# Kernel tuning notes

Measured on AMD Instinct MI355X. Metric: run time of the kernel, lower is better.

## Reference

```python
import jax, jax.numpy as jnp
import numpy as np

NUM_NODES = 100
WINDOW = 128
GH = 256       # graph_hidden_channels
DH = 64        # discrepancy_hidden_channels
OUT = 128      # out_channels
B = 256        # graphs per batch
N = B * NUM_NODES
E = 409600


def _mconv(x, w, b):
    # x: [B, n, W], w: [n, 2, k], b: [n, 2]  (per-node Conv1d(1,2,k), 'same' padding)
    k = w.shape[-1]
    W = x.shape[-1]
    p = k // 2
    xp = jnp.pad(x, ((0, 0), (0, 0), (p, p)))
    win = jnp.stack([xp[..., j:j + W] for j in range(k)], axis=-1)  # [B,n,W,k]
    return jnp.einsum('bnwk,nck->bncw', win, w) + b[None, :, :, None]


def _gcn(x, edge_index, Wg, bg):
    # PyG GCNConv: add self-loops, symmetric normalization, then linear
    Nn = x.shape[0]
    xw = x @ Wg.T
    loops = jnp.arange(Nn, dtype=edge_index.dtype)
    src = jnp.concatenate([edge_index[0], loops])
    dst = jnp.concatenate([edge_index[1], loops])
    deg = jax.ops.segment_sum(jnp.ones(src.shape[0], dtype=xw.dtype), dst, num_segments=Nn)
    norm = jax.lax.rsqrt(jnp.maximum(deg, 1e-12))
    coef = norm[src] * norm[dst]
    agg = jax.ops.segment_sum(coef[:, None] * xw[src], dst, num_segments=Nn)
    return agg + bg


def setup_inputs() -> dict:
    key = jax.random.key(0)
    ks = jax.random.split(key, 20)
    f = 6 * WINDOW
    s = lambda d: 1.0 / np.sqrt(d)
    inp = {
        'x1': jax.random.normal(ks[0], (N, WINDOW), jnp.float32),
        'x2': jax.random.normal(ks[1], (N, WINDOW), jnp.float32),
        'edge_index1': jax.random.randint(ks[2], (2, E), 0, N, jnp.int32),
        'edge_index2': jax.random.randint(ks[3], (2, E), 0, N, jnp.int32),
        'w3': jax.random.normal(ks[4], (NUM_NODES, 2, 3), jnp.float32) * s(3),
        'b3': jax.random.normal(ks[5], (NUM_NODES, 2), jnp.float32) * s(3),
        'w5': jax.random.normal(ks[6], (NUM_NODES, 2, 5), jnp.float32) * s(5),
        'b5': jax.random.normal(ks[7], (NUM_NODES, 2), jnp.float32) * s(5),
        'w7': jax.random.normal(ks[8], (NUM_NODES, 2, 7), jnp.float32) * s(7),
        'b7': jax.random.normal(ks[9], (NUM_NODES, 2), jnp.float32) * s(7),
        'Wff': jax.random.normal(ks[10], (NUM_NODES, GH, f), jnp.float32) * s(f),
        'bff': jax.random.normal(ks[11], (NUM_NODES, GH), jnp.float32) * s(f),
        'Wg': jax.random.normal(ks[12], (GH, GH), jnp.float32) * s(GH),
        'bg': jax.random.normal(ks[13], (GH,), jnp.float32) * s(GH),
        'Wd': jax.random.normal(ks[14], (NUM_NODES, DH, 2 * GH), jnp.float32) * s(2 * GH),
        'bd': jax.random.normal(ks[15], (NUM_NODES, DH), jnp.float32) * s(2 * GH),
        'Wfc': jax.random.normal(ks[16], (OUT, NUM_NODES * DH), jnp.float32) * s(NUM_NODES * DH),
        'bfc': jax.random.normal(ks[17], (OUT,), jnp.float32) * s(NUM_NODES * DH),
    }
    return inp


def reference(x1, x2, edge_index1, edge_index2, w3, b3, w5, b5, w7, b7,
              Wff, bff, Wg, bg, Wd, bd, Wfc, bfc):
    n = w3.shape[0]
    Nn, W = x1.shape
    Bg = Nn // n

    def branch(x):
        xg = x.reshape(Bg, n, W)
        # multiscale CNN: concat conv3/conv5/conv7 along channel -> [B,n,6,W]
        c = jnp.concatenate([_mconv(xg, w3, b3), _mconv(xg, w5, b5), _mconv(xg, w7, b7)], axis=2)
        c = jax.nn.relu(c.reshape(Bg, n, 6 * W))            # channel-major flatten (matches view(-1))
        h = jax.nn.relu(jnp.einsum('bnf,nhf->bnh', c, Wff) + bff)
        return h.reshape(Nn, -1)

    h1 = jax.nn.relu(_gcn(branch(x1), edge_index1, Wg, bg))
    h2 = jax.nn.relu(_gcn(branch(x2), edge_index2, Wg, bg))
    H = h1.shape[-1]
    cat = jnp.concatenate([h1.reshape(Bg, n, H), h2.reshape(Bg, n, H)], axis=-1)  # [B,n,2H]
    d = jnp.einsum('bnf,ndf->bnd', cat, Wd) + bd            # per-node discrepancy FC
    du = jax.nn.relu(d.reshape(Bg, -1))                     # node-major -> [B, n*DH]
    return du @ Wfc.T + bfc
```

## Files before the change

kernel.cpp:

```cpp
#include <hip/hip_runtime.h>

#define DI __device__ __forceinline__

typedef __bf16 bf16_t;
typedef bf16_t bf16x8 __attribute__((ext_vector_type(8)));
typedef float f32x4 __attribute__((ext_vector_type(4)));
typedef ushort ushort8v __attribute__((ext_vector_type(8)));

static constexpr int NNODE = 100, WIN = 128, GH = 256, DH = 64, OUTC = 128, NB = 256;
static constexpr int NTOT = NB * NNODE;
static constexpr int NE = 409600;
static constexpr int FFK = 6 * WIN;
static constexpr size_t CB = (size_t)NNODE * NB * FFK;
static constexpr size_t HB = (size_t)NTOT * GH;
static constexpr int CVT_BLKS = 23264;
static constexpr int NSEG = 64, SEGE = NE / NSEG;
static constexpr int NPK = NTOT / 2;

DI ushort f2bf(float f) {
  union { float f; unsigned u; } v; v.f = f;
  unsigned r = v.u + 0x7fffu + ((v.u >> 16) & 1u);
  return (ushort)(r >> 16);
}
DI float bf2f(ushort s) {
  union { unsigned u; float f; } v; v.u = ((unsigned)s) << 16; return v.f;
}

DI void gload16(const void* g, void* l) {
  __builtin_amdgcn_global_load_lds((const __attribute__((address_space(1))) void*)g,
                                   (__attribute__((address_space(3))) void*)l, 16, 0, 0);
}


DI void cvt_body(int bx, const float* s0, const float* s1, const float* s2, const float* s3,
                 ushort* d0, ushort* d1, ushort* d2, ushort* d3) {
  int j = bx * 256 + threadIdx.x;
  const float* s; ushort* d;
  if (j < 19660800 / 4) { s = s0; d = d0; }
  else if ((j -= 19660800 / 4) < 3276800 / 4) { s = s1; d = d1; }
  else if ((j -= 3276800 / 4) < 819200 / 4) { s = s2; d = d2; }
  else { j -= 819200 / 4; s = s3; d = d3; }
  float4 v = reinterpret_cast<const float4*>(s)[j];
  ushort4 o;
  o.x = f2bf(v.x); o.y = f2bf(v.y); o.z = f2bf(v.z); o.w = f2bf(v.w);
  reinterpret_cast<ushort4*>(d)[j] = o;
}

DI void histseg_body(int bx, const int* e1d, const int* e2d,
                     ushort* rank_local, uint* segcnt, uint* cnt ) {
  int set = bx & 1, seg = bx >> 1;
  int tid = threadIdx.x;
#pragma unroll
  for (int k = 0; k < NPK / 256; ++k) cnt[tid + k * 256] = 0;
  __syncthreads();
  const int* dstp = (set ? e2d : e1d) + seg * SEGE;
  ushort* rl = rank_local + set * NE + seg * SEGE;
#pragma unroll
  for (int k = 0; k < SEGE / 256; ++k) {
    int i = k * 256 + tid;
    int d = dstp[i];
    uint sh = (d & 1) * 16;
    uint old = atomicAdd(&cnt[d >> 1], 1u << sh);
    rl[i] = (ushort)((old >> sh) & 0xffffu);
  }
  __syncthreads();
  uint* sc = segcnt + (size_t)(set * NSEG + seg) * NPK;
#pragma unroll
  for (int k = 0; k < NPK / 256; ++k) sc[tid + k * 256] = cnt[tid + k * 256];
}

DI void fill_body(int bx, const int* e1, const int* e2, const int* offs,
                  const ushort* rank_local, const uint* segbase, int* csr) {
  int i = bx * 256 + threadIdx.x;
  int set = i >= NE;
  int ii = i - set * NE;
  const int* e = set ? e2 : e1;
  int d = e[NE + ii];
  int seg = ii / SEGE;
  uint b32 = segbase[(size_t)(set * NSEG + seg) * NPK + (d >> 1)];
  int base = (b32 >> ((d & 1) * 16)) & 0xffff;
  int pos = offs[set * (NTOT + 1) + d] + base + rank_local[i];
  csr[set * NE + pos] = e[ii];
}

DI void scan_body(int set, const int* deg_, int* offs_, float* norm_) {
  const int* deg = deg_ + set * NTOT;
  int* offs = offs_ + set * (NTOT + 1);
  float* norm = norm_ + set * NTOT;
  __shared__ int part[256];
  int t = threadIdx.x;
  int base = t * 100;
  int s = 0;
  for (int j = 0; j < 100; ++j) s += deg[base + j];
  part[t] = s;
  __syncthreads();
  for (int d = 1; d < 256; d <<= 1) {
    int vv = (t >= d) ? part[t - d] : 0;
    __syncthreads();
    part[t] += vv;
    __syncthreads();
  }
  int run = (t > 0) ? part[t - 1] : 0;
  for (int j = 0; j < 100; ++j) {
    int dv = deg[base + j];
    offs[base + j] = run;
    norm[base + j] = rsqrtf((float)(dv + 1));
    run += dv;
  }
  if (t == 255) offs[NTOT] = part[255];
}

DI void conv_body(int bx, const float* x1, const float* x2,
                  const float* w3, const float* b3, const float* w5, const float* b5,
                  const float* w7, const float* b7, ushort* c, float* xs ) {
  const int t = threadIdx.x;
  const int rowi = t >> 4;
  const int idx = t & 15;
  int r = bx * 16 + rowi;
  int br = r >= NTOT;
  int rr = r - br * NTOT;
  const float* x = br ? x2 : x1;
  int b = rr / 100, node = rr - b * 100;

  float* row = xs + rowi * 136;
  const int w0 = idx * 8;
  float4 v0 = *reinterpret_cast<const float4*>(x + (size_t)rr * WIN + w0);
  float4 v1 = *reinterpret_cast<const float4*>(x + (size_t)rr * WIN + w0 + 4);
  *reinterpret_cast<float4*>(&row[4 + w0]) = v0;
  *reinterpret_cast<float4*>(&row[4 + w0 + 4]) = v1;
  if (idx == 0) { row[0] = 0.f; row[1] = 0.f; row[2] = 0.f; row[3] = 0.f; }
  if (idx == 15) { row[132] = 0.f; row[133] = 0.f; row[134] = 0.f; row[135] = 0.f; }
  __syncthreads();

  float xv[14];
#pragma unroll
  for (int j = 0; j < 14; ++j) xv[j] = row[1 + w0 + j];

  const float* W3 = w3 + node * 6;  const float* B3 = b3 + node * 2;
  const float* W5 = w5 + node * 10; const float* B5 = b5 + node * 2;
  const float* W7 = w7 + node * 14; const float* B7 = b7 + node * 2;
  ushort* out = c + (size_t)br * CB + (size_t)(node * NB + b) * FFK + w0;

#pragma unroll
  for (int ch = 0; ch < 2; ++ch) {
    float k3[3], k5[5], k7[7];
#pragma unroll
    for (int j = 0; j < 3; ++j) k3[j] = W3[ch * 3 + j];
#pragma unroll
    for (int j = 0; j < 5; ++j) k5[j] = W5[ch * 5 + j];
#pragma unroll
    for (int j = 0; j < 7; ++j) k7[j] = W7[ch * 7 + j];
    float bb3 = B3[ch], bb5 = B5[ch], bb7 = B7[ch];
    ushort8v o3, o5, o7;
#pragma unroll
    for (int p = 0; p < 8; ++p) {
      float a3 = bb3, a5 = bb5, a7 = bb7;
#pragma unroll
      for (int j = 0; j < 3; ++j) a3 += k3[j] * xv[p + 2 + j];
#pragma unroll
      for (int j = 0; j < 5; ++j) a5 += k5[j] * xv[p + 1 + j];
#pragma unroll
      for (int j = 0; j < 7; ++j) a7 += k7[j] * xv[p + j];
      o3[p] = f2bf(fmaxf(a3, 0.f));
      o5[p] = f2bf(fmaxf(a5, 0.f));
      o7[p] = f2bf(fmaxf(a7, 0.f));
    }
    *reinterpret_cast<ushort8v*>(out + (0 + ch) * WIN) = o3;
    *reinterpret_cast<ushort8v*>(out + (2 + ch) * WIN) = o5;
    *reinterpret_cast<ushort8v*>(out + (4 + ch) * WIN) = o7;
  }
}

template <int MODE>
DI void gemm_body(int bx, int by, const ushort* __restrict__ A, const ushort* __restrict__ A2,
                  const ushort* __restrict__ Bm, ushort* __restrict__ obf,
                  float* __restrict__ of, const float* __restrict__ bias) {
  constexpr int BN = (MODE == 2) ? 64 : 128;
  constexpr int KT = (MODE == 0) ? 12 : (MODE == 1) ? 4 : (MODE == 2) ? 8 : 4;
  constexpr int LDA = (MODE == 0) ? 768 : (MODE == 1) ? 256 : (MODE == 2) ? 256 : 6400;
  constexpr int LDB = (MODE == 0) ? 768 : (MODE == 1) ? 256 : (MODE == 2) ? 512 : 6400;
  constexpr int MF = (MODE == 2) ? 2 : 4;
  constexpr int NF = 4;

  __shared__ ushort As[128 * 64];
  __shared__ ushort Bs[BN * 64];

  const int tid = threadIdx.x, wv = tid >> 6, lane = tid & 63;
  const int j8 = (((lane & 7) ^ (lane >> 3)) - (lane & 7)) * 8;

  int mt = 0, nt = 0, node = 0, kbase = 0, br = 0;
  if constexpr (MODE == 0) {
    int h = bx;
    int s = (h & 7) * 100 + (h >> 3);
    nt = s & 1; int rest = s >> 1;
    mt = rest & 1; int yy = rest >> 1;
    br = yy >= 100; node = yy - br * 100;
  } else if constexpr (MODE == 1) {
    int h = bx;
    int s = (h & 7) * 100 + (h >> 3);
    nt = s & 1; int rest = s >> 1;
    br = rest >= 200; mt = rest - br * 200;
  } else if constexpr (MODE == 2) { mt = bx; node = by; }
  else { mt = bx; kbase = by * 256; }

  const ushort* Ab = nullptr; const ushort* Bb = nullptr;
  if constexpr (MODE == 0) { Ab = A + (size_t)br * CB + (size_t)node * (NB * FFK) + (size_t)mt * 128 * FFK;
                             Bb = Bm + (size_t)node * (GH * FFK) + (size_t)nt * 128 * FFK; }
  else if constexpr (MODE == 1) { Ab = A + (size_t)br * HB + (size_t)mt * 128 * GH;
                                  Bb = Bm + (size_t)nt * 128 * GH; }
  else if constexpr (MODE == 2) { Bb = Bm + (size_t)node * (DH * 512); }
  else { Ab = A + (size_t)mt * 128 * 6400 + kbase; Bb = Bm + kbase; }

  const int wr = (MODE == 2) ? wv : (wv >> 1);
  const int wc = (MODE == 2) ? 0 : (wv & 1);

  f32x4 acc[MF][NF] = {};

  for (int kt = 0; kt < KT; ++kt) {
    const int k0 = kt * 64;
    __syncthreads();
#pragma unroll
    for (int it = 0; it < 4; ++it) {
      int rb = it * 32 + wv * 8;
      int row = rb + (lane >> 3);
      const ushort* gp;
      if constexpr (MODE == 2) {
        int b_ = mt * 128 + row;
        const ushort* src = (k0 < 256) ? A : A2;
        gp = src + (size_t)(b_ * NNODE + node) * GH + (k0 & 255) + (lane & 7) * 8 + j8;
      } else {
        gp = Ab + (size_t)row * LDA + k0 + (lane & 7) * 8 + j8;
      }
      gload16(gp, &As[rb * 64]);
    }
#pragma unroll
    for (int it = 0; it < BN / 32; ++it) {
      int rb = it * 32 + wv * 8;
      int row = rb + (lane >> 3);
      gload16(Bb + (size_t)row * LDB + k0 + (lane & 7) * 8 + j8, &Bs[rb * 64]);
    }
    __syncthreads();
#pragma unroll
    for (int kk = 0; kk < 2; ++kk) {
      const int ch8 = ((kk * 4 + (lane >> 4)) ^ (lane & 7)) * 8;
      bf16x8 af[MF], bfr[NF];
#pragma unroll
      for (int m = 0; m < MF; ++m) {
        int rr = wr * (MF * 16) + m * 16 + (lane & 15);
        af[m] = *reinterpret_cast<const bf16x8*>(&As[rr * 64 + ch8]);
      }
#pragma unroll
      for (int n = 0; n < NF; ++n) {
        int rr = wc * 64 + n * 16 + (lane & 15);
        bfr[n] = *reinterpret_cast<const bf16x8*>(&Bs[rr * 64 + ch8]);
      }
#pragma unroll
      for (int m = 0; m < MF; ++m)
#pragma unroll
        for (int n = 0; n < NF; ++n)
          acc[m][n] = __builtin_amdgcn_mfma_f32_16x16x32_bf16(af[m], bfr[n], acc[m][n], 0, 0, 0);
    }
  }

  const int lrow = (lane >> 4) * 4, lcol = lane & 15;
#pragma unroll
  for (int m = 0; m < MF; ++m) {
#pragma unroll
    for (int n = 0; n < NF; ++n) {
      int cc = wc * 64 + n * 16 + lcol;
#pragma unroll
      for (int rg = 0; rg < 4; ++rg) {
        int rr = wr * (MF * 16) + m * 16 + lrow + rg;
        float val = acc[m][n][rg];
        if constexpr (MODE == 0) {
          int b_ = mt * 128 + rr;
          int col = nt * 128 + cc;
          val = fmaxf(val + bias[node * GH + col], 0.f);
          obf[(size_t)br * HB + (size_t)(b_ * NNODE + node) * GH + col] = f2bf(val);
        } else if constexpr (MODE == 1) {
          int R = mt * 128 + rr;
          int col = nt * 128 + cc;
          obf[(size_t)br * HB + (size_t)R * GH + col] = f2bf(val * bias[br * NTOT + R]);
        } else if constexpr (MODE == 2) {
          int b_ = mt * 128 + rr;
          val = fmaxf(val + bias[node * DH + cc], 0.f);
          obf[(size_t)b_ * (NNODE * DH) + node * DH + cc] = f2bf(val);
        } else {
          int R = mt * 128 + rr;
          if (by == 0) val += bias[cc];
          atomicAdd(&of[R * OUTC + cc], val);
        }
      }
    }
  }
}


__global__ __launch_bounds__(256) void fused1_k(
    const float* __restrict__ Wff, const float* __restrict__ Wd,
    const float* __restrict__ Wfc, const float* __restrict__ Wg,
    ushort* __restrict__ Wffb, ushort* __restrict__ Wdb,
    ushort* __restrict__ Wfcb, ushort* __restrict__ Wgb,
    const int* __restrict__ e1d, const int* __restrict__ e2d,
    ushort* __restrict__ rank_local, uint* __restrict__ segcnt,
    const float* __restrict__ x1, const float* __restrict__ x2,
    const float* __restrict__ w3, const float* __restrict__ b3,
    const float* __restrict__ w5, const float* __restrict__ b5,
    const float* __restrict__ w7, const float* __restrict__ b7,
    ushort* __restrict__ c) {
  __shared__ uint smem[NPK];
  int bx = blockIdx.x;
  if (bx < 128) histseg_body(bx, e1d, e2d, rank_local, segcnt, smem);
  else if (bx < 3328) conv_body(bx - 128, x1, x2, w3, b3, w5, b5, w7, b7, c, (float*)smem);
  else cvt_body(bx - 3328, Wff, Wd, Wfc, Wg, Wffb, Wdb, Wfcb, Wgb);
}

__global__ __launch_bounds__(256) void segscan_k(const uint* __restrict__ segcnt,
                                                 uint* __restrict__ segbase, int* __restrict__ deg) {
  int set = blockIdx.y;
  int p = blockIdx.x * 256 + threadIdx.x;
  uint lo = 0, hi = 0;
  const uint* sc = segcnt + (size_t)set * NSEG * NPK + p;
  uint* sb = segbase + (size_t)set * NSEG * NPK + p;
  for (int s = 0; s < NSEG; ++s) {
    uint v = sc[(size_t)s * NPK];
    sb[(size_t)s * NPK] = lo | (hi << 16);
    lo += v & 0xffffu; hi += v >> 16;
  }
  reinterpret_cast<int2*>(deg)[set * NPK + p] = make_int2((int)lo, (int)hi);
}

__global__ __launch_bounds__(256) void scan_k(const int* __restrict__ deg,
                                              int* __restrict__ offs, float* __restrict__ nrm) {
  scan_body(blockIdx.x, deg, offs, nrm);
}

__global__ __launch_bounds__(256) void fused3_k(
    const ushort* __restrict__ cbuf, const ushort* __restrict__ Wffb,
    ushort* __restrict__ h, const float* __restrict__ bff,
    const int* __restrict__ e1, const int* __restrict__ e2,
    const int* __restrict__ offs, const ushort* __restrict__ rank_local,
    const uint* __restrict__ segbase, int* __restrict__ csr) {
  if ((int)blockIdx.x < 800)
    gemm_body<0>(blockIdx.x, 0, cbuf, nullptr, Wffb, h, nullptr, bff);
  else
    fill_body(blockIdx.x - 800, e1, e2, offs, rank_local, segbase, csr);
}

template <int MODE>
__global__ __launch_bounds__(256) void gemm_k(const ushort* __restrict__ A, const ushort* __restrict__ A2,
                                              const ushort* __restrict__ Bm, ushort* __restrict__ obf,
                                              float* __restrict__ of, const float* __restrict__ bias) {
  gemm_body<MODE>(blockIdx.x, blockIdx.y, A, A2, Bm, obf, of, bias);
}

__global__ __launch_bounds__(256) void agg_k(const ushort* __restrict__ xw_, const int* __restrict__ offs_,
                                             const int* __restrict__ csr_, const float* __restrict__ norm_,
                                             const float* __restrict__ bg, ushort* __restrict__ hg_) {
  int idx = blockIdx.x * 4 + (threadIdx.x >> 6);
  int br = idx >= NTOT;
  int v = idx - br * NTOT;
  const ushort* xw = xw_ + (size_t)br * HB;
  const int* offs = offs_ + br * (NTOT + 1);
  const int* csr = csr_ + br * NE;
  const float* norm = norm_ + br * NTOT;
  ushort* hg = hg_ + (size_t)br * HB;

  int lane = threadIdx.x & 63;
  int half = lane >> 5;
  int colb = (lane & 31) * 8;
  const ushort* base = xw + colb;

  float a[8] = {0.f, 0.f, 0.f, 0.f, 0.f, 0.f, 0.f, 0.f};
  if (half == 0) {
    ushort8v q = *reinterpret_cast<const ushort8v*>(base + (size_t)v * GH);
#pragma unroll
    for (int i = 0; i < 8; ++i) a[i] += bf2f(q[i]);
  }
  int e0 = offs[v], e1 = offs[v + 1];
  int j = e0 + half;
  for (; j + 6 < e1; j += 8) {
    int s0 = csr[j], s1 = csr[j + 2], s2 = csr[j + 4], s3 = csr[j + 6];
    ushort8v q0 = *reinterpret_cast<const ushort8v*>(base + (size_t)s0 * GH);
    ushort8v q1 = *reinterpret_cast<const ushort8v*>(base + (size_t)s1 * GH);
    ushort8v q2 = *reinterpret_cast<const ushort8v*>(base + (size_t)s2 * GH);
    ushort8v q3 = *reinterpret_cast<const ushort8v*>(base + (size_t)s3 * GH);
#pragma unroll
    for (int i = 0; i < 8; ++i)
      a[i] += (bf2f(q0[i]) + bf2f(q1[i])) + (bf2f(q2[i]) + bf2f(q3[i]));
  }
  for (; j + 2 < e1; j += 4) {
    int s0 = csr[j], s1 = csr[j + 2];
    ushort8v q0 = *reinterpret_cast<const ushort8v*>(base + (size_t)s0 * GH);
    ushort8v q1 = *reinterpret_cast<const ushort8v*>(base + (size_t)s1 * GH);
#pragma unroll
    for (int i = 0; i < 8; ++i) a[i] += bf2f(q0[i]) + bf2f(q1[i]);
  }
  if (j < e1) {
    int s0 = csr[j];
    ushort8v q0 = *reinterpret_cast<const ushort8v*>(base + (size_t)s0 * GH);
#pragma unroll
    for (int i = 0; i < 8; ++i) a[i] += bf2f(q0[i]);
  }
#pragma unroll
  for (int i = 0; i < 8; ++i) a[i] += __shfl_xor(a[i], 32);

  if (half == 0) {
    float nv = norm[v];
    float4 bb0 = *reinterpret_cast<const float4*>(bg + colb);
    float4 bb1 = *reinterpret_cast<const float4*>(bg + colb + 4);
    ushort8v o;
    o[0] = f2bf(fmaxf(nv * a[0] + bb0.x, 0.f));
    o[1] = f2bf(fmaxf(nv * a[1] + bb0.y, 0.f));
    o[2] = f2bf(fmaxf(nv * a[2] + bb0.z, 0.f));
    o[3] = f2bf(fmaxf(nv * a[3] + bb0.w, 0.f));
    o[4] = f2bf(fmaxf(nv * a[4] + bb1.x, 0.f));
    o[5] = f2bf(fmaxf(nv * a[5] + bb1.y, 0.f));
    o[6] = f2bf(fmaxf(nv * a[6] + bb1.z, 0.f));
    o[7] = f2bf(fmaxf(nv * a[7] + bb1.w, 0.f));
    *reinterpret_cast<ushort8v*>(hg + (size_t)v * GH + colb) = o;
  }
}

extern "C" void kernel_launch(void* const* d_in, const int* in_sizes, int n_in,
                              void* d_out, int out_size, void* d_ws, size_t ws_size,
                              hipStream_t stream) {
  const float* x1 = (const float*)d_in[0];
  const float* x2 = (const float*)d_in[1];
  const int* e1 = (const int*)d_in[2];
  const int* e2 = (const int*)d_in[3];
  const float* w3 = (const float*)d_in[4];  const float* b3 = (const float*)d_in[5];
  const float* w5 = (const float*)d_in[6];  const float* b5 = (const float*)d_in[7];
  const float* w7 = (const float*)d_in[8];  const float* b7 = (const float*)d_in[9];
  const float* Wff = (const float*)d_in[10]; const float* bff = (const float*)d_in[11];
  const float* Wg = (const float*)d_in[12];  const float* bg = (const float*)d_in[13];
  const float* Wd = (const float*)d_in[14];  const float* bd = (const float*)d_in[15];
  const float* Wfc = (const float*)d_in[16]; const float* bfc = (const float*)d_in[17];
  float* out = (float*)d_out;

  char* ws = (char*)d_ws;
  size_t off = 0;
  auto alloc = [&](size_t bytes) -> char* {
    char* p = ws + off;
    off = (off + bytes + 255) & ~(size_t)255;
    return p;
  };
  ushort* Wffb = (ushort*)alloc(19660800ull * 2);
  ushort* Wdb  = (ushort*)alloc(3276800ull * 2);
  ushort* Wfcb = (ushort*)alloc(819200ull * 2);
  ushort* Wgb  = (ushort*)alloc(65536ull * 2);
  ushort* cbuf = (ushort*)alloc(2 * CB * 2);
  ushort* h    = (ushort*)alloc(2 * HB * 2);
  ushort* xw   = (ushort*)alloc(2 * HB * 2);
  int* deg     = (int*)alloc(2 * NTOT * 4);
  int* offs    = (int*)alloc(2 * (NTOT + 1) * 4);
  ushort* rankl = (ushort*)alloc(2 * NE * 2);
  uint* segcnt  = (uint*)alloc((size_t)2 * NSEG * NPK * 4);
  uint* segbase = (uint*)alloc((size_t)2 * NSEG * NPK * 4);
  int* csr     = (int*)alloc(2 * NE * 4);
  float* nrm   = (float*)alloc(2 * NTOT * 4);
  ushort* du = cbuf;

  hipMemsetAsync(out, 0, (size_t)out_size * 4, stream);

  fused1_k<<<128 + 3200 + CVT_BLKS, 256, 0, stream>>>(
      Wff, Wd, Wfc, Wg, Wffb, Wdb, Wfcb, Wgb,
      e1 + NE, e2 + NE, rankl, segcnt,
      x1, x2, w3, b3, w5, b5, w7, b7, cbuf);
  segscan_k<<<dim3(NPK / 256, 2), 256, 0, stream>>>(segcnt, segbase, deg);
  scan_k<<<2, 256, 0, stream>>>(deg, offs, nrm);
  fused3_k<<<4000, 256, 0, stream>>>(cbuf, Wffb, h, bff, e1, e2, offs, rankl, segbase, csr);

  gemm_k<1><<<800, 256, 0, stream>>>(h, nullptr, Wgb, xw, nullptr, nrm);
  agg_k<<<12800, 256, 0, stream>>>(xw, offs, csr, nrm, bg, h);

  gemm_k<2><<<dim3(2, 100), 256, 0, stream>>>(h, h + HB, Wdb, du, nullptr, bd);
  gemm_k<3><<<dim3(2, 25), 256, 0, stream>>>(du, nullptr, Wfcb, nullptr, out, bfc);
}
```

Measured before the change: 252.1 us.

## Split GCN aggregation into column slices with half-wave per node

The aggregation kernel now splits the 256 feature columns into four 64-column slices handled by separate blocks, each half-wave processing one node with 4-byte gathers instead of 16-byte gathers split across two half-waves. Block indexing interleaves the branch and slice so neighboring blocks share the same node range, aiming for better L2 locality and more parallelism per edge list. The cost is re-reading CSR indices four times and much narrower memory transactions per gathered row.

```diff
diff --git a/kernel.cpp b/kernel.cpp
--- a/kernel.cpp
+++ b/kernel.cpp
@@ -357,69 +357,47 @@
 __global__ __launch_bounds__(256) void agg_k(const ushort* __restrict__ xw_, const int* __restrict__ offs_,
                                              const int* __restrict__ csr_, const float* __restrict__ norm_,
                                              const float* __restrict__ bg, ushort* __restrict__ hg_) {
-  int idx = blockIdx.x * 4 + (threadIdx.x >> 6);
-  int br = idx >= NTOT;
-  int v = idx - br * NTOT;
+  int bid = blockIdx.x;
+  int c = bid & 7;
+  int i = bid >> 3;
+  int br = c >> 2, slice = c & 3;
+  int hw = threadIdx.x >> 5;
+  int v = i * 8 + hw;
+  int l = threadIdx.x & 31;
+  int col = slice * 64 + l * 2;
+
   const ushort* xw = xw_ + (size_t)br * HB;
   const int* offs = offs_ + br * (NTOT + 1);
   const int* csr = csr_ + br * NE;
   const float* norm = norm_ + br * NTOT;
   ushort* hg = hg_ + (size_t)br * HB;
-
-  int lane = threadIdx.x & 63;
-  int half = lane >> 5;
-  int colb = (lane & 31) * 8;
-  const ushort* base = xw + colb;
-
-  float a[8] = {0.f, 0.f, 0.f, 0.f, 0.f, 0.f, 0.f, 0.f};
-  if (half == 0) {
-    ushort8v q = *reinterpret_cast<const ushort8v*>(base + (size_t)v * GH);
-#pragma unroll
-    for (int i = 0; i < 8; ++i) a[i] += bf2f(q[i]);
-  }
-  int e0 = offs[v], e1 = offs[v + 1];
-  int j = e0 + half;
-  for (; j + 6 < e1; j += 8) {
-    int s0 = csr[j], s1 = csr[j + 2], s2 = csr[j + 4], s3 = csr[j + 6];
-    ushort8v q0 = *reinterpret_cast<const ushort8v*>(base + (size_t)s0 * GH);
-    ushort8v q1 = *reinterpret_cast<const ushort8v*>(base + (size_t)s1 * GH);
-    ushort8v q2 = *reinterpret_cast<const ushort8v*>(base + (size_t)s2 * GH);
-    ushort8v q3 = *reinterpret_cast<const ushort8v*>(base + (size_t)s3 * GH);
-#pragma unroll
-    for (int i = 0; i < 8; ++i)
-      a[i] += (bf2f(q0[i]) + bf2f(q1[i])) + (bf2f(q2[i]) + bf2f(q3[i]));
-  }
-  for (; j + 2 < e1; j += 4) {
-    int s0 = csr[j], s1 = csr[j + 2];
-    ushort8v q0 = *reinterpret_cast<const ushort8v*>(base + (size_t)s0 * GH);
-    ushort8v q1 = *reinterpret_cast<const ushort8v*>(base + (size_t)s1 * GH);
-#pragma unroll
-    for (int i = 0; i < 8; ++i) a[i] += bf2f(q0[i]) + bf2f(q1[i]);
-  }
-  if (j < e1) {
+  const ushort* base = xw + col;
+
+  ushort2 qs = *reinterpret_cast<const ushort2*>(base + (size_t)v * GH);
+  float a0 = bf2f(qs.x), a1 = bf2f(qs.y);
+
+  int e0 = offs[v], e1v = offs[v + 1];
+  int j = e0;
+  for (; j + 3 < e1v; j += 4) {
+    int s0 = csr[j], s1 = csr[j + 1], s2 = csr[j + 2], s3 = csr[j + 3];
+    ushort2 q0 = *reinterpret_cast<const ushort2*>(base + (size_t)s0 * GH);
+    ushort2 q1 = *reinterpret_cast<const ushort2*>(base + (size_t)s1 * GH);
+    ushort2 q2 = *reinterpret_cast<const ushort2*>(base + (size_t)s2 * GH);
+    ushort2 q3 = *reinterpret_cast<const ushort2*>(base + (size_t)s3 * GH);
+    a0 += (bf2f(q0.x) + bf2f(q1.x)) + (bf2f(q2.x) + bf2f(q3.x));
+    a1 += (bf2f(q0.y) + bf2f(q1.y)) + (bf2f(q2.y) + bf2f(q3.y));
+  }
+  for (; j < e1v; ++j) {
     int s0 = csr[j];
-    ushort8v q0 = *reinterpret_cast<const ushort8v*>(base + (size_t)s0 * GH);
-#pragma unroll
-    for (int i = 0; i < 8; ++i) a[i] += bf2f(q0[i]);
-  }
-#pragma unroll
-  for (int i = 0; i < 8; ++i) a[i] += __shfl_xor(a[i], 32);
-
-  if (half == 0) {
-    float nv = norm[v];
-    float4 bb0 = *reinterpret_cast<const float4*>(bg + colb);
-    float4 bb1 = *reinterpret_cast<const float4*>(bg + colb + 4);
-    ushort8v o;
-    o[0] = f2bf(fmaxf(nv * a[0] + bb0.x, 0.f));
-    o[1] = f2bf(fmaxf(nv * a[1] + bb0.y, 0.f));
-    o[2] = f2bf(fmaxf(nv * a[2] + bb0.z, 0.f));
-    o[3] = f2bf(fmaxf(nv * a[3] + bb0.w, 0.f));
-    o[4] = f2bf(fmaxf(nv * a[4] + bb1.x, 0.f));
-    o[5] = f2bf(fmaxf(nv * a[5] + bb1.y, 0.f));
-    o[6] = f2bf(fmaxf(nv * a[6] + bb1.z, 0.f));
-    o[7] = f2bf(fmaxf(nv * a[7] + bb1.w, 0.f));
-    *reinterpret_cast<ushort8v*>(hg + (size_t)v * GH + colb) = o;
-  }
+    ushort2 q0 = *reinterpret_cast<const ushort2*>(base + (size_t)s0 * GH);
+    a0 += bf2f(q0.x); a1 += bf2f(q0.y);
+  }
+
+  float nv = norm[v];
+  ushort2 o;
+  o.x = f2bf(fmaxf(nv * a0 + bg[col], 0.f));
+  o.y = f2bf(fmaxf(nv * a1 + bg[col + 1], 0.f));
+  *reinterpret_cast<ushort2*>(hg + (size_t)v * GH + col) = o;
 }
 
 extern "C" void kernel_launch(void* const* d_in, const int* in_sizes, int n_in,
@@ -472,7 +450,7 @@
   fused3_k<<<4000, 256, 0, stream>>>(cbuf, Wffb, h, bff, e1, e2, offs, rankl, segbase, csr);
 
   gemm_k<1><<<800, 256, 0, stream>>>(h, nullptr, Wgb, xw, nullptr, nrm);
-  agg_k<<<12800, 256, 0, stream>>>(xw, offs, csr, nrm, bg, h);
+  agg_k<<<25600, 256, 0, stream>>>(xw, offs, csr, nrm, bg, h);
 
   gemm_k<2><<<dim3(2, 100), 256, 0, stream>>>(h, h + HB, Wdb, du, nullptr, bd);
   gemm_k<3><<<dim3(2, 25), 256, 0, stream>>>(du, nullptr, Wfcb, nullptr, out, bfc);
```

After: 276.4 us. 1.1x slower.
